# Kernel tuning notes

Measured on AMD Instinct MI355X. Metric: run time of the kernel, lower is better.

Reference implementation:

```python
import math
import jax, jax.numpy as jnp
import numpy as np

N, M = 2048, 128            # fine grid points, coarse points
IN_NF, H, LMAX = 256, 128, 2
A2B = 1.88973
MIN_STD = 0.32 * A2B / 2.0  # two stddevs reach min covalent radius (Bohr)
MAX_STD = 2.32 * A2B / 2.0


def _sph_lmax2(d):
    # norm-normalized real spherical harmonics (e3nn convention), unit input d[..., 3]
    x, y, z = d[..., 0], d[..., 1], d[..., 2]
    s3 = math.sqrt(3.0)
    sh0 = jnp.ones_like(x)[..., None]                                    # [., 1]
    sh1 = jnp.stack([x, y, z], axis=-1)                                  # [., 3]
    sh2 = jnp.stack([s3 * x * z, s3 * x * y,
                     y * y - 0.5 * (x * x + z * z),
                     s3 * y * z, 0.5 * s3 * (z * z - x * x)], axis=-1)   # [., 5]
    return [sh0, sh1, sh2]


def _radial(dist, nb):
    # Gaussian radial basis; two stddevs span [MIN_COV_RAD, MAX_COV_RAD]
    s = jnp.linspace(MIN_STD, MAX_STD, nb, dtype=dist.dtype)
    temps = 2.0 * s * s
    x2 = dist[..., None] ** 2
    return jnp.exp(-x2 / temps) * (2.0 / 3.0) * x2 / temps / (math.pi * temps) ** 1.5


def setup_inputs():
    key = jax.random.key(0)
    k = jax.random.split(key, 10)
    xav = math.sqrt(6.0 / (H + H))
    return {
        'h': jax.random.normal(k[0], (N, IN_NF), jnp.float32),
        'grid_coords': jax.random.normal(k[1], (N, 3), jnp.float32),
        'coarse_coords': jax.random.normal(k[2], (M, 3), jnp.float32),
        'grid_weights': jax.random.uniform(k[3], (N,), jnp.float32),
        'W_pre': jax.random.normal(k[4], (IN_NF, H), jnp.float32) * math.sqrt(2.0 / (IN_NF + H)),
        'b_pre': jnp.zeros((H,), jnp.float32),
        'W_down': jax.random.uniform(k[5], (LMAX + 1, H, H), jnp.float32, -xav, xav),
        'W_up': jax.random.uniform(k[6], (LMAX + 1, H, H), jnp.float32, -xav, xav),
        'W_post': jax.random.normal(k[7], (H, H), jnp.float32) * math.sqrt(2.0 / (H + H)),
        'b_post': jnp.zeros((H,), jnp.float32),
    }


def reference(h, grid_coords, coarse_coords, grid_weights,
              W_pre, b_pre, W_down, W_up, W_post, b_post):
    h = jax.nn.silu(h @ W_pre + b_pre)                            # [N, H]
    # all-pairs directions/distances (vect_cdist); radius_cutoff = inf -> every pair is an edge
    dvec = grid_coords[:, None, :] - coarse_coords[None, :, :]    # [N, M, 3]
    dist = jnp.sqrt((dvec * dvec + 1e-20).sum(-1))                # [N, M]
    dirs = dvec / dist[..., None]
    sh = _sph_lmax2(dirs)                                         # list of [N, M, 2l+1]
    rad = _radial(dist, H)                                        # [N, M, H]
    # tp_down: paths (0e x le -> le); l=0 uses the scalar branch (no 1/sqrt(2l+1))
    # radial gating per hidden channel + quadrature integration onto coarse nodes
    coarse = []
    for l in range(LMAX + 1):
        norm = 1.0 if l == 0 else math.sqrt(2 * l + 1)
        c = jnp.einsum('nu,uw,nmj,nmw,n->mwj',
                       h, W_down[l], sh[l], rad, grid_weights) / norm
        coarse.append(c)                                          # [M, H, 2l+1]
    # tp_up: paths (le x le -> 0e); l>0 branch divides by sqrt(2l+1); scatter back to grid
    out = 0.0
    for l in range(LMAX + 1):
        norm = 1.0 if l == 0 else math.sqrt(2 * l + 1)
        out = out + jnp.einsum('mui,uw,nmi->nw', coarse[l], W_up[l], sh[l]) / norm
    return jax.nn.silu(out @ W_post + b_post)                     # [N, H]
```

## Files before the change

### kernel.cpp

```cpp
#include <hip/hip_runtime.h>
#include <math.h>

#define N_PTS 2048
#define M_PTS 128
#define INNF  256
#define H     128

#define MIN_STDC 0.30235680f
#define MAX_STDC 2.19208680f
#define PI_F     3.14159265358979f
#define LOG2E_F  1.44269504089f

static __device__ __forceinline__ float silu_f(float x) {
  return x / (1.0f + __expf(-x));
}

__global__ __launch_bounds__(256) void k_pre(const float* __restrict__ h,
    const float* __restrict__ W_pre, const float* __restrict__ b_pre,
    const float* __restrict__ W_down, const float* __restrict__ gw,
    float* __restrict__ hdg4) {
  __shared__ float h_lds[4 * INNF];
  __shared__ float hp_lds[4 * H];
  int t = threadIdx.x;
  int n0 = blockIdx.x * 4;
  int w  = t & 127;
  int nh = t >> 7;

  {
    int row = t >> 6, col = (t & 63) << 2;
    float4 v = *(const float4*)(h + (size_t)(n0 + row) * INNF + col);
    *(float4*)&h_lds[row * INNF + col] = v;
  }
  __syncthreads();

  float acc[2] = {0.0f, 0.0f};
  for (int u = 0; u < INNF; u += 8) {
    float4 a0a = *(const float4*)&h_lds[(nh*2 + 0) * INNF + u];
    float4 a0b = *(const float4*)&h_lds[(nh*2 + 0) * INNF + u + 4];
    float4 a1a = *(const float4*)&h_lds[(nh*2 + 1) * INNF + u];
    float4 a1b = *(const float4*)&h_lds[(nh*2 + 1) * INNF + u + 4];
    float wv[8];
    #pragma unroll
    for (int i = 0; i < 8; ++i) wv[i] = W_pre[(u + i)*H + w];
    acc[0] += a0a.x*wv[0] + a0a.y*wv[1] + a0a.z*wv[2] + a0a.w*wv[3]
            + a0b.x*wv[4] + a0b.y*wv[5] + a0b.z*wv[6] + a0b.w*wv[7];
    acc[1] += a1a.x*wv[0] + a1a.y*wv[1] + a1a.z*wv[2] + a1a.w*wv[3]
            + a1b.x*wv[4] + a1b.y*wv[5] + a1b.z*wv[6] + a1b.w*wv[7];
  }
  float bb = b_pre[w];
  hp_lds[(nh*2 + 0)*H + w] = silu_f(acc[0] + bb);
  hp_lds[(nh*2 + 1)*H + w] = silu_f(acc[1] + bb);
  __syncthreads();

  const float stp = (MAX_STDC - MIN_STDC) / 127.0f;
  float s = MIN_STDC + (float)w * stp;
  float temps = 2.0f * s * s;
  float coef = (2.0f/3.0f) / (temps * powf(PI_F * temps, 1.5f));
  float gwv[2] = {gw[n0 + nh*2], gw[n0 + nh*2 + 1]};
  const float invn1 = 0.57735026919f, invn2 = 0.44721359550f;

  float a2[3][2] = {};
  for (int u = 0; u < H; u += 4) {
    float4 p0 = *(const float4*)&hp_lds[(nh*2 + 0)*H + u];
    float4 p1 = *(const float4*)&hp_lds[(nh*2 + 1)*H + u];
    #pragma unroll
    for (int l = 0; l < 3; ++l) {
      float w0 = W_down[((size_t)l*H + u + 0)*H + w];
      float w1 = W_down[((size_t)l*H + u + 1)*H + w];
      float w2 = W_down[((size_t)l*H + u + 2)*H + w];
      float w3 = W_down[((size_t)l*H + u + 3)*H + w];
      a2[l][0] += p0.x*w0 + p0.y*w1 + p0.z*w2 + p0.w*w3;
      a2[l][1] += p1.x*w0 + p1.y*w1 + p1.z*w2 + p1.w*w3;
    }
  }
  #pragma unroll
  for (int r = 0; r < 2; ++r) {
    float sc = gwv[r] * coef;
    size_t base = ((size_t)(n0 + nh*2 + r) * H + w) * 4;
    hdg4[base + 0] = a2[0][r]*sc;
    hdg4[base + 1] = a2[1][r]*sc*invn1;
    hdg4[base + 2] = a2[2][r]*sc*invn2;
    hdg4[base + 3] = 0.0f;
  }
}

__global__ __launch_bounds__(256) void k_down(const float* __restrict__ gc,
    const float* __restrict__ cc, const float* __restrict__ hdg4,
    float* __restrict__ c_part) {
  __shared__ float lds[4608];
  int t = threadIdx.x;
  int m0 = blockIdx.x * 4;
  int ss = blockIdx.y;
  int n0 = ss * 64;
  int w  = t & 127;
  int nh = t >> 7;

  {
    int n_loc = t >> 2, m_loc = t & 3;
    int n = n0 + n_loc, m = m0 + m_loc;
    float dx = gc[3*n]   - cc[3*m];
    float dy = gc[3*n+1] - cc[3*m+1];
    float dz = gc[3*n+2] - cc[3*m+2];
    float d2 = dx*dx + dy*dy + dz*dz + 3e-20f;
    float inv = rsqrtf(d2);
    float x = dx*inv, y = dy*inv, z = dz*inv;
    const float s3 = 1.73205080757f;
    float* dst = &lds[(size_t)t * 12];
    dst[0] = 1.0f; dst[1] = x; dst[2] = y; dst[3] = z;
    dst[4] = s3*x*z; dst[5] = s3*x*y; dst[6] = y*y - 0.5f*(x*x + z*z);
    dst[7] = s3*y*z; dst[8] = 0.5f*s3*(z*z - x*x);
    dst[9] = d2; dst[10] = 0.0f; dst[11] = 0.0f;
  }
  __syncthreads();

  const float stp = (MAX_STDC - MIN_STDC) / 127.0f;
  float sw = MIN_STDC + (float)w * stp;
  float nl2t = LOG2E_F / (2.0f * sw * sw);

  float acc[4][9] = {};
  for (int j = 0; j < 32; j += 4) {
    float4 hv[4];
    #pragma unroll
    for (int q = 0; q < 4; ++q)
      hv[q] = *(const float4*)(hdg4 + ((size_t)(n0 + nh*32 + j + q)*H + w)*4);
    #pragma unroll
    for (int q = 0; q < 4; ++q) {
      const float* shb = &lds[(size_t)(nh*32 + j + q) * 48];
      #pragma unroll
      for (int mm = 0; mm < 4; ++mm) {
        float4 q0 = *(const float4*)(shb + mm*12);
        float4 q1 = *(const float4*)(shb + mm*12 + 4);
        float4 q2 = *(const float4*)(shb + mm*12 + 8);
        float e  = exp2f(-q2.y * nl2t);
        float rp = e * q2.y;
        float t0 = hv[q].x*rp, t1 = hv[q].y*rp, t2 = hv[q].z*rp;
        acc[mm][0] += t0;
        acc[mm][1] += t1*q0.y; acc[mm][2] += t1*q0.z; acc[mm][3] += t1*q0.w;
        acc[mm][4] += t2*q1.x; acc[mm][5] += t2*q1.y;
        acc[mm][6] += t2*q1.z; acc[mm][7] += t2*q1.w;
        acc[mm][8] += t2*q2.x;
      }
    }
  }

  __syncthreads();
  if (nh == 1) {
    #pragma unroll
    for (int mm = 0; mm < 4; ++mm)
      #pragma unroll
      for (int li = 0; li < 9; ++li)
        lds[(mm*9 + li)*128 + w] = acc[mm][li];
  }
  __syncthreads();
  if (nh == 0) {
    #pragma unroll
    for (int mm = 0; mm < 4; ++mm)
      #pragma unroll
      for (int li = 0; li < 9; ++li) {
        float v = acc[mm][li] + lds[(mm*9 + li)*128 + w];
        c_part[(((size_t)ss*M_PTS + m0 + mm)*9 + li)*H + w] = v;
      }
  }
}

__global__ __launch_bounds__(256) void k_cu(const float* __restrict__ c_part,
    const float* __restrict__ W_up, float* __restrict__ CU9) {
  __shared__ float c_lds[H * 12];
  __shared__ float red[9 * H];
  int t = threadIdx.x, m = blockIdx.x;
  int w = t & 127, uh = t >> 7;

  for (int idx = t; idx < 9 * H; idx += 256) {
    int li = idx >> 7, u = idx & 127;
    float v = 0.0f;
    #pragma unroll 8
    for (int s = 0; s < 32; ++s)
      v += c_part[(((size_t)s*M_PTS + m)*9 + li)*H + u];
    c_lds[u*12 + li] = v;
  }
  __syncthreads();

  float acc[9] = {};
  for (int u = uh*64; u < uh*64 + 64; ++u) {
    float4 q0 = *(const float4*)&c_lds[u*12];
    float4 q1 = *(const float4*)&c_lds[u*12 + 4];
    float  q8 = c_lds[u*12 + 8];
    float w0 = W_up[((size_t)0*H + u)*H + w];
    float w1 = W_up[((size_t)1*H + u)*H + w];
    float w2 = W_up[((size_t)2*H + u)*H + w];
    acc[0] += q0.x*w0;
    acc[1] += q0.y*w1; acc[2] += q0.z*w1; acc[3] += q0.w*w1;
    acc[4] += q1.x*w2; acc[5] += q1.y*w2; acc[6] += q1.z*w2;
    acc[7] += q1.w*w2; acc[8] += q8*w2;
  }
  __syncthreads();
  if (uh == 1) {
    #pragma unroll
    for (int li = 0; li < 9; ++li) red[li*128 + w] = acc[li];
  }
  __syncthreads();
  if (uh == 0) {
    const float invn[3] = {1.0f, 0.57735026919f, 0.44721359550f};
    #pragma unroll
    for (int li = 0; li < 9; ++li) {
      int l = (li == 0) ? 0 : (li < 4 ? 1 : 2);
      CU9[((size_t)m*9 + li)*H + w] = (acc[li] + red[li*128 + w]) * invn[l];
    }
  }
}

__global__ __launch_bounds__(256) void k_up(const float* __restrict__ gc,
    const float* __restrict__ cc, const float* __restrict__ CU9,
    float* __restrict__ out_part) {
  __shared__ float At[36 * 34];
  __shared__ float Bl[36 * 128];
  int t = threadIdx.x;
  int n0 = blockIdx.x * 32;
  int ks = blockIdx.y;
  int tgn = t >> 4;
  int w0 = (t & 15) * 8;
  float acc[2][8] = {};

  for (int ch = 0; ch < 2; ++ch) {
    int m0 = ks*8 + ch*4;
    __syncthreads();
    if (t < 128) {
      int n_loc = t >> 2, m_loc = t & 3;
      int n = n0 + n_loc, m = m0 + m_loc;
      float dx = gc[3*n]   - cc[3*m];
      float dy = gc[3*n+1] - cc[3*m+1];
      float dz = gc[3*n+2] - cc[3*m+2];
      float d2 = dx*dx + dy*dy + dz*dz + 3e-20f;
      float inv = rsqrtf(d2);
      float x = dx*inv, y = dy*inv, z = dz*inv;
      const float s3 = 1.73205080757f;
      float sh[9];
      sh[0] = 1.0f; sh[1] = x; sh[2] = y; sh[3] = z;
      sh[4] = s3*x*z; sh[5] = s3*x*y; sh[6] = y*y - 0.5f*(x*x + z*z);
      sh[7] = s3*y*z; sh[8] = 0.5f*s3*(z*z - x*x);
      #pragma unroll
      for (int li = 0; li < 9; ++li)
        At[(m_loc*9 + li)*34 + n_loc] = sh[li];
    }
    #pragma unroll
    for (int i = 0; i < 5; ++i) {
      int idx = t + i*256;
      if (idx < 1152)
        *(float4*)&Bl[idx*4] = *(const float4*)(CU9 + ((size_t)m0*9)*H + idx*4);
    }
    __syncthreads();
    #pragma unroll 6
    for (int k = 0; k < 36; ++k) {
      float2 a = *(const float2*)&At[k*34 + 2*tgn];
      float4 b0 = *(const float4*)&Bl[k*128 + w0];
      float4 b1 = *(const float4*)&Bl[k*128 + w0 + 4];
      float bv[8] = {b0.x, b0.y, b0.z, b0.w, b1.x, b1.y, b1.z, b1.w};
      #pragma unroll
      for (int c = 0; c < 8; ++c) {
        acc[0][c] += a.x * bv[c];
        acc[1][c] += a.y * bv[c];
      }
    }
  }
  #pragma unroll
  for (int r = 0; r < 2; ++r) {
    size_t row = (size_t)ks*N_PTS + n0 + 2*tgn + r;
    *(float4*)(out_part + row*H + w0)     = make_float4(acc[r][0], acc[r][1], acc[r][2], acc[r][3]);
    *(float4*)(out_part + row*H + w0 + 4) = make_float4(acc[r][4], acc[r][5], acc[r][6], acc[r][7]);
  }
}

__global__ __launch_bounds__(256) void k_post(const float* __restrict__ out_part,
    const float* __restrict__ W_post, const float* __restrict__ b_post,
    float* __restrict__ out) {
  __shared__ float op[4 * H];
  int t = threadIdx.x;
  int n0 = blockIdx.x * 4;
  int w = t & 127, nh = t >> 7;

  #pragma unroll
  for (int i = 0; i < 2; ++i) {
    int idx = t + i*256;
    int nl = idx >> 7, ww = idx & 127;
    float v = 0.0f;
    #pragma unroll
    for (int s = 0; s < 16; ++s)
      v += out_part[((size_t)s*N_PTS + n0 + nl)*H + ww];
    op[nl*H + ww] = v;
  }
  __syncthreads();

  float acc[2] = {0.0f, 0.0f};
  for (int u = 0; u < H; u += 4) {
    float4 p0 = *(const float4*)&op[(nh*2 + 0)*H + u];
    float4 p1 = *(const float4*)&op[(nh*2 + 1)*H + u];
    float w0 = W_post[(u+0)*H + w];
    float w1 = W_post[(u+1)*H + w];
    float w2 = W_post[(u+2)*H + w];
    float w3 = W_post[(u+3)*H + w];
    acc[0] += p0.x*w0 + p0.y*w1 + p0.z*w2 + p0.w*w3;
    acc[1] += p1.x*w0 + p1.y*w1 + p1.z*w2 + p1.w*w3;
  }
  float bp = b_post[w];
  out[(size_t)(n0 + nh*2 + 0)*H + w] = silu_f(acc[0] + bp);
  out[(size_t)(n0 + nh*2 + 1)*H + w] = silu_f(acc[1] + bp);
}

extern "C" void kernel_launch(void* const* d_in, const int* in_sizes, int n_in,
                              void* d_out, int out_size, void* d_ws, size_t ws_size,
                              hipStream_t stream) {
  const float* h      = (const float*)d_in[0];
  const float* gc     = (const float*)d_in[1];
  const float* cc     = (const float*)d_in[2];
  const float* gw     = (const float*)d_in[3];
  const float* W_pre  = (const float*)d_in[4];
  const float* b_pre  = (const float*)d_in[5];
  const float* W_down = (const float*)d_in[6];
  const float* W_up   = (const float*)d_in[7];
  const float* W_post = (const float*)d_in[8];
  const float* b_post = (const float*)d_in[9];

  float* ws       = (float*)d_ws;
  float* hdg4     = ws;
  float* c_part   = hdg4 + 1048576;
  float* CU9      = c_part + 4718592;
  float* out_part = c_part;
  float* out      = (float*)d_out;

  k_pre <<<512,           256, 0, stream>>>(h, W_pre, b_pre, W_down, gw, hdg4);
  k_down<<<dim3(32,32),   256, 0, stream>>>(gc, cc, hdg4, c_part);
  k_cu  <<<128,           256, 0, stream>>>(c_part, W_up, CU9);
  k_up  <<<dim3(64,16),   256, 0, stream>>>(gc, cc, CU9, out_part);
  k_post<<<512,           256, 0, stream>>>(out_part, W_post, b_post, out);
}
```

Measured before the change: 166.1 us.

## Replace split-K partial buffers with atomic accumulation and regrid pre/cu kernels

```diff
diff --git a/kernel.cpp b/kernel.cpp
--- a/kernel.cpp
+++ b/kernel.cpp
@@ -18,75 +18,69 @@
 __global__ __launch_bounds__(256) void k_pre(const float* __restrict__ h,
     const float* __restrict__ W_pre, const float* __restrict__ b_pre,
     const float* __restrict__ W_down, const float* __restrict__ gw,
-    float* __restrict__ hdg4) {
-  __shared__ float h_lds[4 * INNF];
-  __shared__ float hp_lds[4 * H];
-  int t = threadIdx.x;
-  int n0 = blockIdx.x * 4;
+    float* __restrict__ hdg4, float* __restrict__ c4,
+    float* __restrict__ out_pre) {
+  __shared__ float h_lds[2 * INNF];
+  __shared__ float hp_lds[2 * H];
+  int t = threadIdx.x;
+  int b = blockIdx.x;
+  int n0 = b * 2;
   int w  = t & 127;
   int nh = t >> 7;
-
-  {
+  int n  = n0 + nh;
+
+  const float4 z4 = make_float4(0.f, 0.f, 0.f, 0.f);
+  ((float4*)c4)[(size_t)b*144 + t % 144 ] = z4;
+  if (t < 144) ((float4*)c4)[(size_t)b*144 + t] = z4;
+  if (t < 64)  ((float4*)out_pre)[(size_t)b*64 + t] = z4;
+
+  if (t < 128) {
     int row = t >> 6, col = (t & 63) << 2;
-    float4 v = *(const float4*)(h + (size_t)(n0 + row) * INNF + col);
-    *(float4*)&h_lds[row * INNF + col] = v;
-  }
-  __syncthreads();
-
-  float acc[2] = {0.0f, 0.0f};
+    *(float4*)&h_lds[row * INNF + col] =
+        *(const float4*)(h + (size_t)(n0 + row) * INNF + col);
+  }
+  __syncthreads();
+
+  float acc = 0.0f;
   for (int u = 0; u < INNF; u += 8) {
-    float4 a0a = *(const float4*)&h_lds[(nh*2 + 0) * INNF + u];
-    float4 a0b = *(const float4*)&h_lds[(nh*2 + 0) * INNF + u + 4];
-    float4 a1a = *(const float4*)&h_lds[(nh*2 + 1) * INNF + u];
-    float4 a1b = *(const float4*)&h_lds[(nh*2 + 1) * INNF + u + 4];
+    float4 aa = *(const float4*)&h_lds[nh * INNF + u];
+    float4 ab = *(const float4*)&h_lds[nh * INNF + u + 4];
     float wv[8];
     #pragma unroll
     for (int i = 0; i < 8; ++i) wv[i] = W_pre[(u + i)*H + w];
-    acc[0] += a0a.x*wv[0] + a0a.y*wv[1] + a0a.z*wv[2] + a0a.w*wv[3]
-            + a0b.x*wv[4] + a0b.y*wv[5] + a0b.z*wv[6] + a0b.w*wv[7];
-    acc[1] += a1a.x*wv[0] + a1a.y*wv[1] + a1a.z*wv[2] + a1a.w*wv[3]
-            + a1b.x*wv[4] + a1b.y*wv[5] + a1b.z*wv[6] + a1b.w*wv[7];
-  }
-  float bb = b_pre[w];
-  hp_lds[(nh*2 + 0)*H + w] = silu_f(acc[0] + bb);
-  hp_lds[(nh*2 + 1)*H + w] = silu_f(acc[1] + bb);
+    acc += aa.x*wv[0] + aa.y*wv[1] + aa.z*wv[2] + aa.w*wv[3]
+         + ab.x*wv[4] + ab.y*wv[5] + ab.z*wv[6] + ab.w*wv[7];
+  }
+  hp_lds[nh*H + w] = silu_f(acc + b_pre[w]);
   __syncthreads();
 
   const float stp = (MAX_STDC - MIN_STDC) / 127.0f;
   float s = MIN_STDC + (float)w * stp;
   float temps = 2.0f * s * s;
   float coef = (2.0f/3.0f) / (temps * powf(PI_F * temps, 1.5f));
-  float gwv[2] = {gw[n0 + nh*2], gw[n0 + nh*2 + 1]};
+  float gwv = gw[n];
   const float invn1 = 0.57735026919f, invn2 = 0.44721359550f;
 
-  float a2[3][2] = {};
+  float a2[3] = {};
   for (int u = 0; u < H; u += 4) {
-    float4 p0 = *(const float4*)&hp_lds[(nh*2 + 0)*H + u];
-    float4 p1 = *(const float4*)&hp_lds[(nh*2 + 1)*H + u];
+    float4 p = *(const float4*)&hp_lds[nh*H + u];
     #pragma unroll
     for (int l = 0; l < 3; ++l) {
       float w0 = W_down[((size_t)l*H + u + 0)*H + w];
       float w1 = W_down[((size_t)l*H + u + 1)*H + w];
       float w2 = W_down[((size_t)l*H + u + 2)*H + w];
       float w3 = W_down[((size_t)l*H + u + 3)*H + w];
-      a2[l][0] += p0.x*w0 + p0.y*w1 + p0.z*w2 + p0.w*w3;
-      a2[l][1] += p1.x*w0 + p1.y*w1 + p1.z*w2 + p1.w*w3;
+      a2[l] += p.x*w0 + p.y*w1 + p.z*w2 + p.w*w3;
     }
   }
-  #pragma unroll
-  for (int r = 0; r < 2; ++r) {
-    float sc = gwv[r] * coef;
-    size_t base = ((size_t)(n0 + nh*2 + r) * H + w) * 4;
-    hdg4[base + 0] = a2[0][r]*sc;
-    hdg4[base + 1] = a2[1][r]*sc*invn1;
-    hdg4[base + 2] = a2[2][r]*sc*invn2;
-    hdg4[base + 3] = 0.0f;
-  }
+  float sc = gwv * coef;
+  *(float4*)(hdg4 + ((size_t)n * H + w) * 4) =
+      make_float4(a2[0]*sc, a2[1]*sc*invn1, a2[2]*sc*invn2, 0.0f);
 }
 
 __global__ __launch_bounds__(256) void k_down(const float* __restrict__ gc,
     const float* __restrict__ cc, const float* __restrict__ hdg4,
-    float* __restrict__ c_part) {
+    float* __restrict__ c4) {
   __shared__ float lds[4608];
   int t = threadIdx.x;
   int m0 = blockIdx.x * 4;
@@ -115,7 +109,7 @@
 
   const float stp = (MAX_STDC - MIN_STDC) / 127.0f;
   float sw = MIN_STDC + (float)w * stp;
-  float nl2t = LOG2E_F / (2.0f * sw * sw);
+  float m_nl2t = -LOG2E_F / (2.0f * sw * sw);
 
   float acc[4][9] = {};
   for (int j = 0; j < 32; j += 4) {
@@ -131,7 +125,7 @@
         float4 q0 = *(const float4*)(shb + mm*12);
         float4 q1 = *(const float4*)(shb + mm*12 + 4);
         float4 q2 = *(const float4*)(shb + mm*12 + 8);
-        float e  = exp2f(-q2.y * nl2t);
+        float e  = exp2f(q2.y * m_nl2t);
         float rp = e * q2.y;
         float t0 = hv[q].x*rp, t1 = hv[q].y*rp, t2 = hv[q].z*rp;
         acc[mm][0] += t0;
@@ -153,124 +147,102 @@
   }
   __syncthreads();
   if (nh == 0) {
+    int s4 = ss >> 3;
     #pragma unroll
     for (int mm = 0; mm < 4; ++mm)
       #pragma unroll
       for (int li = 0; li < 9; ++li) {
         float v = acc[mm][li] + lds[(mm*9 + li)*128 + w];
-        c_part[(((size_t)ss*M_PTS + m0 + mm)*9 + li)*H + w] = v;
+        atomicAdd(&c4[(((size_t)s4*M_PTS + m0 + mm)*9 + li)*H + w], v);
       }
   }
 }
 
-__global__ __launch_bounds__(256) void k_cu(const float* __restrict__ c_part,
+__global__ __launch_bounds__(128) void k_cu(const float* __restrict__ c4,
     const float* __restrict__ W_up, float* __restrict__ CU9) {
-  __shared__ float c_lds[H * 12];
-  __shared__ float red[9 * H];
-  int t = threadIdx.x, m = blockIdx.x;
-  int w = t & 127, uh = t >> 7;
-
-  for (int idx = t; idx < 9 * H; idx += 256) {
-    int li = idx >> 7, u = idx & 127;
-    float v = 0.0f;
-    #pragma unroll 8
-    for (int s = 0; s < 32; ++s)
-      v += c_part[(((size_t)s*M_PTS + m)*9 + li)*H + u];
-    c_lds[u*12 + li] = v;
-  }
-  __syncthreads();
-
-  float acc[9] = {};
-  for (int u = uh*64; u < uh*64 + 64; ++u) {
-    float4 q0 = *(const float4*)&c_lds[u*12];
-    float4 q1 = *(const float4*)&c_lds[u*12 + 4];
-    float  q8 = c_lds[u*12 + 8];
-    float w0 = W_up[((size_t)0*H + u)*H + w];
-    float w1 = W_up[((size_t)1*H + u)*H + w];
-    float w2 = W_up[((size_t)2*H + u)*H + w];
-    acc[0] += q0.x*w0;
-    acc[1] += q0.y*w1; acc[2] += q0.z*w1; acc[3] += q0.w*w1;
-    acc[4] += q1.x*w2; acc[5] += q1.y*w2; acc[6] += q1.z*w2;
-    acc[7] += q1.w*w2; acc[8] += q8*w2;
-  }
-  __syncthreads();
-  if (uh == 1) {
-    #pragma unroll
-    for (int li = 0; li < 9; ++li) red[li*128 + w] = acc[li];
-  }
-  __syncthreads();
-  if (uh == 0) {
-    const float invn[3] = {1.0f, 0.57735026919f, 0.44721359550f};
-    #pragma unroll
-    for (int li = 0; li < 9; ++li) {
-      int l = (li == 0) ? 0 : (li < 4 ? 1 : 2);
-      CU9[((size_t)m*9 + li)*H + w] = (acc[li] + red[li*128 + w]) * invn[l];
-    }
-  }
+  __shared__ float c_lds[H];
+  int t = threadIdx.x;
+  int m = blockIdx.x, li = blockIdx.y;
+  size_t base = ((size_t)m*9 + li)*H + t;
+  float v = c4[base] + c4[(size_t)1*M_PTS*9*H + base]
+          + c4[(size_t)2*M_PTS*9*H + base] + c4[(size_t)3*M_PTS*9*H + base];
+  c_lds[t] = v;
+  __syncthreads();
+
+  int l = (li == 0) ? 0 : (li < 4 ? 1 : 2);
+  const float invn[3] = {1.0f, 0.57735026919f, 0.44721359550f};
+  float acc = 0.0f;
+  for (int u = 0; u < H; u += 4) {
+    float w0 = W_up[((size_t)l*H + u + 0)*H + t];
+    float w1 = W_up[((size_t)l*H + u + 1)*H + t];
+    float w2 = W_up[((size_t)l*H + u + 2)*H + t];
+    float w3 = W_up[((size_t)l*H + u + 3)*H + t];
+    acc += c_lds[u]*w0 + c_lds[u+1]*w1 + c_lds[u+2]*w2 + c_lds[u+3]*w3;
+  }
+  CU9[((size_t)m*9 + li)*H + t] = acc * invn[l];
 }
 
 __global__ __launch_bounds__(256) void k_up(const float* __restrict__ gc,
     const float* __restrict__ cc, const float* __restrict__ CU9,
-    float* __restrict__ out_part) {
-  __shared__ float At[36 * 34];
-  __shared__ float Bl[36 * 128];
+    float* __restrict__ out_pre) {
+  __shared__ float At[72 * 34];
+  __shared__ float Bl[72 * 128];
   int t = threadIdx.x;
   int n0 = blockIdx.x * 32;
   int ks = blockIdx.y;
   int tgn = t >> 4;
   int w0 = (t & 15) * 8;
+
+  {
+    int ch = t >> 7, idx = t & 127;
+    int n_loc = idx >> 2, m_loc = idx & 3;
+    int mrel = ch*4 + m_loc;
+    int n = n0 + n_loc, m = ks*8 + mrel;
+    float dx = gc[3*n]   - cc[3*m];
+    float dy = gc[3*n+1] - cc[3*m+1];
+    float dz = gc[3*n+2] - cc[3*m+2];
+    float d2 = dx*dx + dy*dy + dz*dz + 3e-20f;
+    float inv = rsqrtf(d2);
+    float x = dx*inv, y = dy*inv, z = dz*inv;
+    const float s3 = 1.73205080757f;
+    float sh[9];
+    sh[0] = 1.0f; sh[1] = x; sh[2] = y; sh[3] = z;
+    sh[4] = s3*x*z; sh[5] = s3*x*y; sh[6] = y*y - 0.5f*(x*x + z*z);
+    sh[7] = s3*y*z; sh[8] = 0.5f*s3*(z*z - x*x);
+    #pragma unroll
+    for (int li = 0; li < 9; ++li)
+      At[(mrel*9 + li)*34 + n_loc] = sh[li];
+  }
+  #pragma unroll
+  for (int i = 0; i < 9; ++i) {
+    int idx = t + i*256;
+    *(float4*)&Bl[idx*4] = *(const float4*)(CU9 + (size_t)ks*72*H + idx*4);
+  }
+  __syncthreads();
+
   float acc[2][8] = {};
-
-  for (int ch = 0; ch < 2; ++ch) {
-    int m0 = ks*8 + ch*4;
-    __syncthreads();
-    if (t < 128) {
-      int n_loc = t >> 2, m_loc = t & 3;
-      int n = n0 + n_loc, m = m0 + m_loc;
-      float dx = gc[3*n]   - cc[3*m];
-      float dy = gc[3*n+1] - cc[3*m+1];
-      float dz = gc[3*n+2] - cc[3*m+2];
-      float d2 = dx*dx + dy*dy + dz*dz + 3e-20f;
-      float inv = rsqrtf(d2);
-      float x = dx*inv, y = dy*inv, z = dz*inv;
-      const float s3 = 1.73205080757f;
-      float sh[9];
-      sh[0] = 1.0f; sh[1] = x; sh[2] = y; sh[3] = z;
-      sh[4] = s3*x*z; sh[5] = s3*x*y; sh[6] = y*y - 0.5f*(x*x + z*z);
-      sh[7] = s3*y*z; sh[8] = 0.5f*s3*(z*z - x*x);
-      #pragma unroll
-      for (int li = 0; li < 9; ++li)
-        At[(m_loc*9 + li)*34 + n_loc] = sh[li];
-    }
-    #pragma unroll
-    for (int i = 0; i < 5; ++i) {
-      int idx = t + i*256;
-      if (idx < 1152)
-        *(float4*)&Bl[idx*4] = *(const float4*)(CU9 + ((size_t)m0*9)*H + idx*4);
-    }
-    __syncthreads();
-    #pragma unroll 6
-    for (int k = 0; k < 36; ++k) {
-      float2 a = *(const float2*)&At[k*34 + 2*tgn];
-      float4 b0 = *(const float4*)&Bl[k*128 + w0];
-      float4 b1 = *(const float4*)&Bl[k*128 + w0 + 4];
-      float bv[8] = {b0.x, b0.y, b0.z, b0.w, b1.x, b1.y, b1.z, b1.w};
-      #pragma unroll
-      for (int c = 0; c < 8; ++c) {
-        acc[0][c] += a.x * bv[c];
-        acc[1][c] += a.y * bv[c];
-      }
+  #pragma unroll 8
+  for (int k = 0; k < 72; ++k) {
+    float2 a = *(const float2*)&At[k*34 + 2*tgn];
+    float4 b0 = *(const float4*)&Bl[k*128 + w0];
+    float4 b1 = *(const float4*)&Bl[k*128 + w0 + 4];
+    float bv[8] = {b0.x, b0.y, b0.z, b0.w, b1.x, b1.y, b1.z, b1.w};
+    #pragma unroll
+    for (int c = 0; c < 8; ++c) {
+      acc[0][c] += a.x * bv[c];
+      acc[1][c] += a.y * bv[c];
     }
   }
   #pragma unroll
   for (int r = 0; r < 2; ++r) {
-    size_t row = (size_t)ks*N_PTS + n0 + 2*tgn + r;
-    *(float4*)(out_part + row*H + w0)     = make_float4(acc[r][0], acc[r][1], acc[r][2], acc[r][3]);
-    *(float4*)(out_part + row*H + w0 + 4) = make_float4(acc[r][4], acc[r][5], acc[r][6], acc[r][7]);
-  }
-}
-
-__global__ __launch_bounds__(256) void k_post(const float* __restrict__ out_part,
+    float* dst = out_pre + (size_t)(n0 + 2*tgn + r)*H + w0;
+    #pragma unroll
+    for (int c = 0; c < 8; ++c)
+      atomicAdd(dst + c, acc[r][c]);
+  }
+}
+
+__global__ __launch_bounds__(256) void k_post(const float* __restrict__ out_pre,
     const float* __restrict__ W_post, const float* __restrict__ b_post,
     float* __restrict__ out) {
   __shared__ float op[4 * H];
@@ -278,15 +250,10 @@
   int n0 = blockIdx.x * 4;
   int w = t & 127, nh = t >> 7;
 
-  #pragma unroll
-  for (int i = 0; i < 2; ++i) {
-    int idx = t + i*256;
-    int nl = idx >> 7, ww = idx & 127;
-    float v = 0.0f;
-    #pragma unroll
-    for (int s = 0; s < 16; ++s)
-      v += out_part[((size_t)s*N_PTS + n0 + nl)*H + ww];
-    op[nl*H + ww] = v;
+  if (t < 128) {
+    int row = t >> 5, col = (t & 31) << 2;
+    *(float4*)&op[row*H + col] =
+        *(const float4*)(out_pre + (size_t)(n0 + row)*H + col);
   }
   __syncthreads();
 
@@ -322,14 +289,15 @@
 
   float* ws       = (float*)d_ws;
   float* hdg4     = ws;
-  float* c_part   = hdg4 + 1048576;
-  float* CU9      = c_part + 4718592;
-  float* out_part = c_part;
+  float* c4       = hdg4 + 1048576;
+  float* CU9      = c4 + 589824;
+  float* out_pre  = CU9 + 147456;
   float* out      = (float*)d_out;
 
-  k_pre <<<512,           256, 0, stream>>>(h, W_pre, b_pre, W_down, gw, hdg4);
-  k_down<<<dim3(32,32),   256, 0, stream>>>(gc, cc, hdg4, c_part);
-  k_cu  <<<128,           256, 0, stream>>>(c_part, W_up, CU9);
-  k_up  <<<dim3(64,16),   256, 0, stream>>>(gc, cc, CU9, out_part);
-  k_post<<<512,           256, 0, stream>>>(out_part, W_post, b_post, out);
-}
+  k_pre <<<1024,          256, 0, stream>>>(h, W_pre, b_pre, W_down, gw,
+                                            hdg4, c4, out_pre);
+  k_down<<<dim3(32,32),   256, 0, stream>>>(gc, cc, hdg4, c4);
+  k_cu  <<<dim3(128,9),   128, 0, stream>>>(c4, W_up, CU9);
+  k_up  <<<dim3(64,16),   256, 0, stream>>>(gc, cc, CU9, out_pre);
+  k_post<<<512,           256, 0, stream>>>(out_pre, W_post, b_post, out);
+}
```

Result: slower. 261.6 us (+57.5%).
